# Kernel optimization log

Hardware: AMD Instinct MI355X
Metric: run time of the kernel (lower is better)

The kernel has to match this reference:

```python
import jax, jax.numpy as jnp
import numpy as np

B, L, D_ENC = 32, 512, 512
STEPS = 32
E_DIM = 128      # embedding_dim
A_DIM = 256      # attention_dim
H = 512          # hidden_size
VOCAB = 32000


def _linear(x, W, b):
    return x @ W.T + b


def setup_inputs() -> dict:
    key = jax.random.key(0)
    ks = jax.random.split(key, 12)
    s = lambda fan_in: 1.0 / np.sqrt(fan_in)
    return {
        "encoder_outputs": jax.random.normal(ks[0], (B, L, D_ENC), dtype=jnp.float32),
        "target_seq": jax.random.randint(ks[1], (B, STEPS), 0, VOCAB, dtype=jnp.int64),
        "pos_embedding": jax.random.normal(ks[2], (STEPS, E_DIM), dtype=jnp.float32),
        "dec_proj_W": jax.random.uniform(ks[3], (A_DIM, E_DIM), minval=-s(E_DIM), maxval=s(E_DIM)),
        "dec_proj_b": jnp.zeros((A_DIM,), jnp.float32),
        "enc_proj_W": jax.random.uniform(ks[4], (A_DIM, D_ENC), minval=-s(D_ENC), maxval=s(D_ENC)),
        "enc_proj_b": jnp.zeros((A_DIM,), jnp.float32),
        "attn_score_W": jax.random.uniform(ks[5], (1, A_DIM), minval=-s(A_DIM), maxval=s(A_DIM)),
        "attn_score_b": jnp.zeros((1,), jnp.float32),
        "hidden_proj_W": jax.random.uniform(ks[6], (H, E_DIM), minval=-s(E_DIM), maxval=s(E_DIM)),
        "hidden_proj_b": jnp.zeros((H,), jnp.float32),
        "fc_out_W": jax.random.uniform(ks[7], (VOCAB, H + D_ENC), minval=-s(H + D_ENC), maxval=s(H + D_ENC)),
        "fc_out_b": jnp.zeros((VOCAB,), jnp.float32),
    }


def reference(encoder_outputs, target_seq, pos_embedding,
              dec_proj_W, dec_proj_b, enc_proj_W, enc_proj_b,
              attn_score_W, attn_score_b, hidden_proj_W, hidden_proj_b,
              fc_out_W, fc_out_b):
    batch = encoder_outputs.shape[0]
    steps = target_seq.shape[1]
    # [B, L, A]
    enc_proj = _linear(encoder_outputs, enc_proj_W, enc_proj_b)
    # [B, S, E]  (dropout=0 in eval)
    pos_emb = jnp.broadcast_to(pos_embedding[:steps][None], (batch, steps, pos_embedding.shape[1]))
    # [B, S, A]
    dec_query = _linear(pos_emb, dec_proj_W, dec_proj_b)
    # additive attention: [B, S, L, A]
    combined = jnp.tanh(enc_proj[:, None, :, :] + dec_query[:, :, None, :])
    # score reduction to scalar: [B, S, L]
    attn_scores = jnp.einsum('bsla,a->bsl', combined, attn_score_W[0]) + attn_score_b[0]
    attn_weights = jax.nn.softmax(attn_scores, axis=2)
    # context: [B, S, D_enc]
    context = jnp.einsum('bsl,bld->bsd', attn_weights, encoder_outputs)
    hidden = _linear(pos_emb, hidden_proj_W, hidden_proj_b)  # [B, S, H]
    logits = _linear(jnp.concatenate([hidden, context], axis=-1), fc_out_W, fc_out_b)
    return logits
```

## Files before the change

kernel.cpp:

```cpp
#include <hip/hip_runtime.h>
#include <hip/hip_bf16.h>
#include <stdint.h>

typedef __attribute__((ext_vector_type(4))) float f32x4;
typedef __attribute__((ext_vector_type(8))) short short8;

#define B_   32
#define L_   512
#define DE_  512
#define S_   32
#define ED_  128
#define AD_  256
#define HD_  512
#define VOC_ 32000
#define M_   1024

__device__ __forceinline__ unsigned short f2bf(float f){
  union { float f; unsigned int u; } v; v.f = f;
  unsigned int u = v.u;
  unsigned int r = (u + 0x7FFFu + ((u >> 16) & 1u)) >> 16;
  return (unsigned short)r;
}

__device__ __forceinline__ float bf2f(unsigned short u){
  union { unsigned int u; float f; } v; v.u = ((unsigned int)u) << 16;
  return v.f;
}

__device__ __forceinline__ float tanh_fast(float x){
  float t = __expf(2.0f * x);
  return (t - 1.0f) * __builtin_amdgcn_rcpf(t + 1.0f);
}

__device__ __forceinline__ void gl_lds16(const void* g, void* l){
  __builtin_amdgcn_global_load_lds(
      (const __attribute__((address_space(1))) unsigned int*)g,
      (__attribute__((address_space(3))) unsigned int*)l, 16, 0, 0);
}

extern "C" __global__ void __launch_bounds__(256)
k_prep(const float* __restrict__ enc, unsigned short* __restrict__ enc_bf,
       const float* __restrict__ eW, unsigned short* __restrict__ encW_bf,
       const float* __restrict__ pos,
       const float* __restrict__ dW, const float* __restrict__ db,
       const float* __restrict__ hW, const float* __restrict__ hb,
       float* __restrict__ dq, unsigned short* __restrict__ hbf){
  int blk = blockIdx.x, tid = threadIdx.x;
  if (blk < 8192){
    int i = blk * 256 + tid;
    f32x4 v = ((const f32x4*)enc)[i];
    ushort4 o;
    o.x = f2bf(v[0]); o.y = f2bf(v[1]); o.z = f2bf(v[2]); o.w = f2bf(v[3]);
    ((ushort4*)enc_bf)[i] = o;
  } else if (blk < 8320){
    int i = (blk - 8192) * 256 + tid;
    f32x4 v = ((const f32x4*)eW)[i];
    ushort4 o;
    o.x = f2bf(v[0]); o.y = f2bf(v[1]); o.z = f2bf(v[2]); o.w = f2bf(v[3]);
    ((ushort4*)encW_bf)[i] = o;
  } else {
    int t = (blk - 8320) * 256 + tid;
    if (t < S_ * AD_){
      int s = t >> 8, a = t & 255;
      const float* p = pos + s * ED_;
      const float* wrow = dW + a * ED_;
      float acc = db[a];
      #pragma unroll 4
      for (int e = 0; e < ED_; ++e) acc += p[e] * wrow[e];
      dq[t] = acc;
    } else if (t < S_ * AD_ + S_ * HD_){
      int u = t - S_ * AD_;
      int s = u >> 9, h = u & 511;
      const float* p = pos + s * ED_;
      const float* wrow = hW + h * ED_;
      float acc = hb[h];
      #pragma unroll 4
      for (int e = 0; e < ED_; ++e) acc += p[e] * wrow[e];
      hbf[u] = f2bf(acc);
    }
  }
}

extern "C" __global__ void __launch_bounds__(256, 4)
k_gemm_encp(const unsigned short* __restrict__ A, const unsigned short* __restrict__ Bt,
            const float* __restrict__ bias, unsigned short* __restrict__ C){
  __shared__ unsigned short As[2][128 * 32];
  __shared__ unsigned short Bs[2][128 * 32];
  int bm = blockIdx.x >> 1, bn = blockIdx.x & 1;
  int tid = threadIdx.x, wid = tid >> 6, lane = tid & 63;
  int fr = lane & 15, fq = lane >> 4;
  int wm = wid >> 1, wn = wid & 1;
  int srow = lane >> 2;
  int scol = ((lane & 3) ^ ((lane >> 3) & 3)) * 8;
  int c0 = wid * 2;
  const unsigned short* aS0 = A  + (size_t)(bm * 128 + c0 * 16 + srow) * 512 + scol;
  const unsigned short* aS1 = aS0 + (size_t)16 * 512;
  const unsigned short* bS0 = Bt + (size_t)(bn * 128 + c0 * 16 + srow) * 512 + scol;
  const unsigned short* bS1 = bS0 + (size_t)16 * 512;
  int swzfq = (fq ^ ((fr >> 1) & 3)) * 8;

  f32x4 acc[4][4];
  #pragma unroll
  for (int i = 0; i < 4; ++i)
    #pragma unroll
    for (int j = 0; j < 4; ++j) acc[i][j] = (f32x4)0.0f;

#define STAGE_E(buf, kk) do { \
    gl_lds16(aS0 + (kk), &As[buf][c0 * 512]); \
    gl_lds16(aS1 + (kk), &As[buf][c0 * 512 + 512]); \
    gl_lds16(bS0 + (kk), &Bs[buf][c0 * 512]); \
    gl_lds16(bS1 + (kk), &Bs[buf][c0 * 512 + 512]); \
  } while (0)

  STAGE_E(0, 0);
  __syncthreads();

  int cur = 0;
  for (int t = 0; t < 16; ++t){
    if (t < 15) STAGE_E(cur ^ 1, (size_t)(t + 1) * 32);
    short8 a[4], b[4];
    #pragma unroll
    for (int mf = 0; mf < 4; ++mf) a[mf] = *(const short8*)&As[cur][(wm * 64 + mf * 16 + fr) * 32 + swzfq];
    #pragma unroll
    for (int nf = 0; nf < 4; ++nf) b[nf] = *(const short8*)&Bs[cur][(wn * 64 + nf * 16 + fr) * 32 + swzfq];
    #pragma unroll
    for (int mf = 0; mf < 4; ++mf)
      #pragma unroll
      for (int nf = 0; nf < 4; ++nf)
        acc[mf][nf] = __builtin_amdgcn_mfma_f32_16x16x32_bf16(a[mf], b[nf], acc[mf][nf], 0, 0, 0);
    __syncthreads();
    cur ^= 1;
  }
#undef STAGE_E

  #pragma unroll
  for (int mf = 0; mf < 4; ++mf){
    int row = bm * 128 + wm * 64 + mf * 16 + fq * 4;
    #pragma unroll
    for (int nf = 0; nf < 4; ++nf){
      int col = bn * 128 + wn * 64 + nf * 16 + fr;
      float bv = bias[col];
      #pragma unroll
      for (int j = 0; j < 4; ++j)
        C[(size_t)(row + j) * 256 + col] = f2bf(acc[mf][nf][j] + bv);
    }
  }
}

extern "C" __global__ void __launch_bounds__(256)
k_mid(const float* __restrict__ fcW, const unsigned short* __restrict__ hbf,
      const float* __restrict__ fcb, unsigned short* __restrict__ Wc,
      float* __restrict__ logh,
      const unsigned short* __restrict__ encp, const float* __restrict__ dq,
      const float* __restrict__ vW, float* __restrict__ wgt){
  int blk = blockIdx.x;
  if (blk < 500){
    int bn = blk;
    int tid = threadIdx.x, wid = tid >> 6, lane = tid & 63;
    int fr = lane & 15, fq = lane >> 4;
    #pragma unroll 8
    for (int i = 0; i < 32; ++i){
      int idx = i * 256 + tid;
      int row = idx >> 7, c4 = idx & 127;
      f32x4 v = *(const f32x4*)&fcW[(size_t)(bn * 64 + row) * 1024 + 512 + c4 * 4];
      ushort4 o;
      o.x = f2bf(v[0]); o.y = f2bf(v[1]); o.z = f2bf(v[2]); o.w = f2bf(v[3]);
      *(ushort4*)&Wc[(size_t)(bn * 64 + row) * 512 + c4 * 4] = o;
    }
    int col = bn * 64 + wid * 16 + fr;
    const float* brow = fcW + (size_t)col * 1024;
    f32x4 acc0 = (f32x4)0.0f, acc1 = (f32x4)0.0f;
    #pragma unroll 4
    for (int k0 = 0; k0 < 512; k0 += 32){
      int ko = k0 + fq * 8;
      f32x4 b0 = *(const f32x4*)(brow + ko);
      f32x4 b1 = *(const f32x4*)(brow + ko + 4);
      short8 bfr;
      bfr[0] = (short)f2bf(b0[0]); bfr[1] = (short)f2bf(b0[1]);
      bfr[2] = (short)f2bf(b0[2]); bfr[3] = (short)f2bf(b0[3]);
      bfr[4] = (short)f2bf(b1[0]); bfr[5] = (short)f2bf(b1[1]);
      bfr[6] = (short)f2bf(b1[2]); bfr[7] = (short)f2bf(b1[3]);
      short8 a0 = *(const short8*)&hbf[(size_t)fr * 512 + ko];
      short8 a1 = *(const short8*)&hbf[(size_t)(16 + fr) * 512 + ko];
      acc0 = __builtin_amdgcn_mfma_f32_16x16x32_bf16(a0, bfr, acc0, 0, 0, 0);
      acc1 = __builtin_amdgcn_mfma_f32_16x16x32_bf16(a1, bfr, acc1, 0, 0, 0);
    }
    float bv = fcb[col];
    #pragma unroll
    for (int j = 0; j < 4; ++j){
      logh[(size_t)(fq * 4 + j) * VOC_ + col]      = acc0[j] + bv;
      logh[(size_t)(16 + fq * 4 + j) * VOC_ + col] = acc1[j] + bv;
    }
  } else {
    int wg = blk - 500;
    int b = wg >> 5, s = wg & 31;
    int tid = threadIdx.x, wid = tid >> 6, lane = tid & 63;
    int half = lane >> 5, a0 = (lane & 31) * 8;
    __shared__ float sc[512];
    __shared__ float redm[4], reds[4];
    f32x4 dqa = *(const f32x4*)&dq[s * AD_ + a0];
    f32x4 dqb = *(const f32x4*)&dq[s * AD_ + a0 + 4];
    f32x4 va  = *(const f32x4*)&vW[a0];
    f32x4 vb  = *(const f32x4*)&vW[a0 + 4];
    for (int it = 0; it < 64; ++it){
      int l = wid * 128 + it * 2 + half;
      short8 e8 = *(const short8*)&encp[((size_t)(b * 512 + l)) * 256 + a0];
      float p = 0.0f;
      #pragma unroll
      for (int j = 0; j < 4; ++j) p += tanh_fast(bf2f((unsigned short)e8[j]) + dqa[j]) * va[j];
      #pragma unroll
      for (int j = 0; j < 4; ++j) p += tanh_fast(bf2f((unsigned short)e8[4 + j]) + dqb[j]) * vb[j];
      #pragma unroll
      for (int off = 16; off >= 1; off >>= 1) p += __shfl_xor(p, off);
      if ((lane & 31) == 0) sc[l] = p;
    }
    __syncthreads();
    float s0 = sc[tid], s1 = sc[tid + 256];
    float m = fmaxf(s0, s1);
    #pragma unroll
    for (int off = 32; off >= 1; off >>= 1) m = fmaxf(m, __shfl_xor(m, off));
    if (lane == 0) redm[wid] = m;
    __syncthreads();
    m = fmaxf(fmaxf(redm[0], redm[1]), fmaxf(redm[2], redm[3]));
    float e0 = __expf(s0 - m), e1 = __expf(s1 - m);
    float sum = e0 + e1;
    #pragma unroll
    for (int off = 32; off >= 1; off >>= 1) sum += __shfl_xor(sum, off);
    if (lane == 0) reds[wid] = sum;
    __syncthreads();
    float tot = reds[0] + reds[1] + reds[2] + reds[3];
    float inv = __builtin_amdgcn_rcpf(tot);
    size_t base = (size_t)(b * 32 + s) * 512;
    wgt[base + tid] = e0 * inv;
    wgt[base + tid + 256] = e1 * inv;
  }
}

extern "C" __global__ void __launch_bounds__(256)
k_ctx(const unsigned short* __restrict__ encb, const float* __restrict__ wgt,
      unsigned short* __restrict__ ctx){
  int b = blockIdx.x >> 4, dt = blockIdx.x & 15;
  int tid = threadIdx.x;
  __shared__ float wl[32 * 512];
  #pragma unroll 8
  for (int i = 0; i < 64; ++i)
    wl[i * 256 + tid] = wgt[(size_t)b * 16384 + i * 256 + tid];
  __syncthreads();
  int d = dt * 32 + (tid & 31);
  int grp = tid >> 5;
  float acc0 = 0, acc1 = 0, acc2 = 0, acc3 = 0;
  const unsigned short* ebase = encb + (size_t)b * 262144 + d;
  const float* w0 = &wl[(grp * 4 + 0) * 512];
  const float* w1 = &wl[(grp * 4 + 1) * 512];
  const float* w2 = &wl[(grp * 4 + 2) * 512];
  const float* w3 = &wl[(grp * 4 + 3) * 512];
  #pragma unroll 8
  for (int l = 0; l < 512; ++l){
    float e = bf2f(ebase[(size_t)l * 512]);
    acc0 += w0[l] * e; acc1 += w1[l] * e; acc2 += w2[l] * e; acc3 += w3[l] * e;
  }
  size_t obase = (size_t)(b * 32 + grp * 4) * 512 + d;
  ctx[obase]        = f2bf(acc0);
  ctx[obase + 512]  = f2bf(acc1);
  ctx[obase + 1024] = f2bf(acc2);
  ctx[obase + 1536] = f2bf(acc3);
}

extern "C" __global__ void __launch_bounds__(512, 4)
k_gemm_main(const unsigned short* __restrict__ Abf, const unsigned short* __restrict__ Wc,
            const float* __restrict__ logh, float* __restrict__ out){
  __shared__ unsigned short As[2][128 * 32];
  __shared__ unsigned short Bs[3][256 * 32];
  int orig = blockIdx.x;
  int wg = (orig & 7) * 125 + (orig >> 3);
  int bm = wg & 7, bn = wg >> 3;
  int tid = threadIdx.x, wid = tid >> 6, lane = tid & 63;
  int fr = lane & 15, fq = lane >> 4;
  int wm = wid >> 2, wn = wid & 3;
  int abase = bm * 128, bbase = bn * 256;
  int srow = lane >> 2;
  int scol = ((lane & 3) ^ ((lane >> 3) & 3)) * 8;
  const unsigned short* aS0 = Abf + (size_t)(abase + wid * 16 + srow) * 512 + scol;
  const unsigned short* bS0 = Wc  + (size_t)(bbase + wid * 32 + srow) * 512 + scol;
  const unsigned short* bS1 = bS0 + (size_t)16 * 512;
  int swzfq = (fq ^ ((fr >> 1) & 3)) * 8;

  f32x4 acc[4][4];
  #pragma unroll
  for (int i = 0; i < 4; ++i)
    #pragma unroll
    for (int jj = 0; jj < 4; ++jj) acc[i][jj] = (f32x4)0.0f;

#define STAGE_A(buf, kk) gl_lds16(aS0 + (kk), &As[buf][wid * 512])
#define STAGE_B(buf, kk) do { \
    gl_lds16(bS0 + (kk), &Bs[buf][wid * 1024]); \
    gl_lds16(bS1 + (kk), &Bs[buf][wid * 1024 + 512]); \
  } while (0)

  STAGE_A(0, 0);
  STAGE_B(0, 0);
  STAGE_B(1, 32);
  asm volatile("s_waitcnt vmcnt(2)" ::: "memory");
  __builtin_amdgcn_s_barrier();
  __builtin_amdgcn_sched_barrier(0);

  #pragma unroll
  for (int t = 0; t < 16; ++t){
    const int ca = t & 1, cb = t % 3;
    short8 a[4], b[4];
    if (t < 15) STAGE_A(ca ^ 1, (size_t)(t + 1) * 32);
    #pragma unroll
    for (int nf = 0; nf < 4; ++nf)
      b[nf] = *(const short8*)&Bs[cb][(wn * 64 + nf * 16 + fr) * 32 + swzfq];
    #pragma unroll
    for (int mf = 0; mf < 2; ++mf)
      a[mf] = *(const short8*)&As[ca][(wm * 64 + mf * 16 + fr) * 32 + swzfq];
    __builtin_amdgcn_s_setprio(1);
    #pragma unroll
    for (int mf = 0; mf < 2; ++mf)
      #pragma unroll
      for (int nf = 0; nf < 4; ++nf)
        acc[mf][nf] = __builtin_amdgcn_mfma_f32_16x16x32_bf16(a[mf], b[nf], acc[mf][nf], 0, 0, 0);
    __builtin_amdgcn_s_setprio(0);
    if (t < 14) STAGE_B((t + 2) % 3, (size_t)(t + 2) * 32);
    #pragma unroll
    for (int mf = 2; mf < 4; ++mf)
      a[mf] = *(const short8*)&As[ca][(wm * 64 + mf * 16 + fr) * 32 + swzfq];
    __builtin_amdgcn_s_setprio(1);
    #pragma unroll
    for (int mf = 2; mf < 4; ++mf)
      #pragma unroll
      for (int nf = 0; nf < 4; ++nf)
        acc[mf][nf] = __builtin_amdgcn_mfma_f32_16x16x32_bf16(a[mf], b[nf], acc[mf][nf], 0, 0, 0);
    __builtin_amdgcn_s_setprio(0);
    if (t < 14)       asm volatile("s_waitcnt vmcnt(2)" ::: "memory");
    else if (t == 14) asm volatile("s_waitcnt vmcnt(0)" ::: "memory");
    if (t < 15){
      __builtin_amdgcn_s_barrier();
      __builtin_amdgcn_sched_barrier(0);
    }
  }
#undef STAGE_A
#undef STAGE_B

  #pragma unroll
  for (int mf = 0; mf < 4; ++mf){
    int rowb = bm * 128 + wm * 64 + mf * 16 + fq * 4;
    #pragma unroll
    for (int nf = 0; nf < 4; ++nf){
      int col = bn * 256 + wn * 64 + nf * 16 + fr;
      #pragma unroll
      for (int jj = 0; jj < 4; ++jj){
        int r = rowb + jj;
        out[(size_t)r * VOC_ + col] = acc[mf][nf][jj] + logh[(size_t)(r & 31) * VOC_ + col];
      }
    }
  }
}

extern "C" void kernel_launch(void* const* d_in, const int* in_sizes, int n_in,
                              void* d_out, int out_size, void* d_ws, size_t ws_size,
                              hipStream_t stream){
  const float* enc = (const float*)d_in[0];
  const float* pos = (const float*)d_in[2];
  const float* dW  = (const float*)d_in[3];
  const float* db  = (const float*)d_in[4];
  const float* eW  = (const float*)d_in[5];
  const float* eb  = (const float*)d_in[6];
  const float* vW  = (const float*)d_in[7];
  const float* hW  = (const float*)d_in[9];
  const float* hb  = (const float*)d_in[10];
  const float* fcW = (const float*)d_in[11];
  const float* fcb = (const float*)d_in[12];
  float* out = (float*)d_out;

  char* w = (char*)d_ws;
  unsigned short* Wc_bf   = (unsigned short*)(w);
  unsigned short* enc_bf  = (unsigned short*)(w + 32768000);
  unsigned short* encp_bf = (unsigned short*)(w + 49545216);
  unsigned short* ctx     = (unsigned short*)(w + 57933824);
  float*          logh    = (float*)(w + 58982400);
  float*          dq      = (float*)(w + 63078400);
  unsigned short* hbf     = (unsigned short*)(w + 63111168);
  unsigned short* encW_bf = (unsigned short*)(w + 63143936);
  float*          wgt     = (float*)(w + 63406080);

  k_prep<<<dim3(8416), dim3(256), 0, stream>>>(enc, enc_bf, eW, encW_bf,
                                               pos, dW, db, hW, hb, dq, hbf);
  k_gemm_encp<<<dim3(256), dim3(256), 0, stream>>>(enc_bf, encW_bf, eb, encp_bf);
  k_mid<<<dim3(1524), dim3(256), 0, stream>>>(fcW, hbf, fcb, Wc_bf, logh,
                                              encp_bf, dq, vW, wgt);
  k_ctx<<<dim3(512), dim3(256), 0, stream>>>(enc_bf, wgt, ctx);
  k_gemm_main<<<dim3(1000), dim3(512), 0, stream>>>(ctx, Wc_bf, logh, out);
}
```

Baseline: 204.5 us.

## Tile attention scores over L-chunks with LDS reuse and split softmax into separate kernel

```diff
diff --git a/kernel.cpp b/kernel.cpp
--- a/kernel.cpp
+++ b/kernel.cpp
@@ -152,7 +152,8 @@
       const float* __restrict__ fcb, unsigned short* __restrict__ Wc,
       float* __restrict__ logh,
       const unsigned short* __restrict__ encp, const float* __restrict__ dq,
-      const float* __restrict__ vW, float* __restrict__ wgt){
+      const float* __restrict__ vW, float* __restrict__ scoreT){
+  __shared__ char smem[49152];
   int blk = blockIdx.x;
   if (blk < 500){
     int bn = blk;
@@ -192,47 +193,88 @@
       logh[(size_t)(16 + fq * 4 + j) * VOC_ + col] = acc1[j] + bv;
     }
   } else {
-    int wg = blk - 500;
-    int b = wg >> 5, s = wg & 31;
-    int tid = threadIdx.x, wid = tid >> 6, lane = tid & 63;
-    int half = lane >> 5, a0 = (lane & 31) * 8;
-    __shared__ float sc[512];
-    __shared__ float redm[4], reds[4];
-    f32x4 dqa = *(const f32x4*)&dq[s * AD_ + a0];
-    f32x4 dqb = *(const f32x4*)&dq[s * AD_ + a0 + 4];
-    f32x4 va  = *(const f32x4*)&vW[a0];
-    f32x4 vb  = *(const f32x4*)&vW[a0 + 4];
-    for (int it = 0; it < 64; ++it){
-      int l = wid * 128 + it * 2 + half;
-      short8 e8 = *(const short8*)&encp[((size_t)(b * 512 + l)) * 256 + a0];
-      float p = 0.0f;
-      #pragma unroll
-      for (int j = 0; j < 4; ++j) p += tanh_fast(bf2f((unsigned short)e8[j]) + dqa[j]) * va[j];
-      #pragma unroll
-      for (int j = 0; j < 4; ++j) p += tanh_fast(bf2f((unsigned short)e8[4 + j]) + dqb[j]) * vb[j];
-      #pragma unroll
-      for (int off = 16; off >= 1; off >>= 1) p += __shfl_xor(p, off);
-      if ((lane & 31) == 0) sc[l] = p;
+    unsigned short* eL = (unsigned short*)smem;
+    float* pp = (float*)(smem + 16384);
+    int blk2 = blk - 500;
+    int b = blk2 >> 4, c = blk2 & 15;
+    int tid = threadIdx.x, w = tid >> 6, lane = tid & 63;
+    #pragma unroll
+    for (int i = 0; i < 4; ++i){
+      int rb = i * 8 + w * 2;
+      gl_lds16(encp + (size_t)(b * 512 + c * 32 + rb + (lane >> 5)) * 256 + (lane & 31) * 8,
+               &eL[rb * 256]);
+    }
+    int s = tid >> 3, g = tid & 7;
+    f32x4 dqv[8], vv[8];
+    #pragma unroll
+    for (int k = 0; k < 8; ++k){
+      dqv[k] = *(const f32x4*)&dq[s * 256 + g * 32 + k * 4];
+      vv[k]  = *(const f32x4*)&vW[g * 32 + k * 4];
     }
     __syncthreads();
-    float s0 = sc[tid], s1 = sc[tid + 256];
-    float m = fmaxf(s0, s1);
-    #pragma unroll
-    for (int off = 32; off >= 1; off >>= 1) m = fmaxf(m, __shfl_xor(m, off));
-    if (lane == 0) redm[wid] = m;
+    #pragma unroll 4
+    for (int l = 0; l < 32; ++l){
+      float a = 0.0f;
+      #pragma unroll
+      for (int k = 0; k < 8; ++k){
+        uint2 e4 = *(const uint2*)&eL[l * 256 + g * 32 + k * 4];
+        a += tanh_fast(bf2f((unsigned short)(e4.x & 0xffff)) + dqv[k][0]) * vv[k][0];
+        a += tanh_fast(bf2f((unsigned short)(e4.x >> 16))    + dqv[k][1]) * vv[k][1];
+        a += tanh_fast(bf2f((unsigned short)(e4.y & 0xffff)) + dqv[k][2]) * vv[k][2];
+        a += tanh_fast(bf2f((unsigned short)(e4.y >> 16))    + dqv[k][3]) * vv[k][3];
+      }
+      pp[l * 256 + tid] = a;
+    }
     __syncthreads();
-    m = fmaxf(fmaxf(redm[0], redm[1]), fmaxf(redm[2], redm[3]));
-    float e0 = __expf(s0 - m), e1 = __expf(s1 - m);
-    float sum = e0 + e1;
-    #pragma unroll
-    for (int off = 32; off >= 1; off >>= 1) sum += __shfl_xor(sum, off);
-    if (lane == 0) reds[wid] = sum;
-    __syncthreads();
-    float tot = reds[0] + reds[1] + reds[2] + reds[3];
-    float inv = __builtin_amdgcn_rcpf(tot);
-    size_t base = (size_t)(b * 32 + s) * 512;
-    wgt[base + tid] = e0 * inv;
-    wgt[base + tid + 256] = e1 * inv;
+    #pragma unroll
+    for (int k2 = 0; k2 < 4; ++k2){
+      int p = tid + k2 * 256;
+      int l = p >> 5, ss = p & 31;
+      f32x4 x0 = *(const f32x4*)&pp[p * 8];
+      f32x4 x1 = *(const f32x4*)&pp[p * 8 + 4];
+      float sum = (x0[0] + x0[1]) + (x0[2] + x0[3]) + ((x1[0] + x1[1]) + (x1[2] + x1[3]));
+      scoreT[((size_t)b * 512 + c * 32 + l) * 32 + ss] = sum;
+    }
+  }
+}
+
+extern "C" __global__ void __launch_bounds__(256)
+k_smax(const float* __restrict__ scoreT, float* __restrict__ wgt){
+  __shared__ float sL[512 * 32];
+  __shared__ float pm[32][8], ps[32][8];
+  __shared__ float Mf[32], invf[32];
+  int b = blockIdx.x, tid = threadIdx.x;
+  for (int idx = tid; idx < 16384; idx += 256){
+    int l = idx >> 5, s2 = idx & 31;
+    sL[l * 32 + (s2 ^ (l & 31))] = scoreT[(size_t)b * 16384 + idx];
+  }
+  __syncthreads();
+  int s2 = tid & 31, part = tid >> 5;
+  float m = -1e30f;
+  for (int l = part * 64; l < part * 64 + 64; ++l)
+    m = fmaxf(m, sL[l * 32 + (s2 ^ (l & 31))]);
+  pm[s2][part] = m;
+  __syncthreads();
+  float M = pm[s2][0];
+  #pragma unroll
+  for (int j2 = 1; j2 < 8; ++j2) M = fmaxf(M, pm[s2][j2]);
+  float sum = 0.0f;
+  for (int l = part * 64; l < part * 64 + 64; ++l)
+    sum += __expf(sL[l * 32 + (s2 ^ (l & 31))] - M);
+  ps[s2][part] = sum;
+  __syncthreads();
+  if (part == 0){
+    float L = ps[s2][0];
+    #pragma unroll
+    for (int j2 = 1; j2 < 8; ++j2) L += ps[s2][j2];
+    Mf[s2] = M;
+    invf[s2] = __builtin_amdgcn_rcpf(L);
+  }
+  __syncthreads();
+  for (int idx = tid; idx < 16384; idx += 256){
+    int ss = idx >> 9, l = idx & 511;
+    float x = sL[l * 32 + (ss ^ (l & 31))];
+    wgt[(size_t)(b * 32 + ss) * 512 + l] = __expf(x - Mf[ss]) * invf[ss];
   }
 }
 
@@ -384,12 +426,14 @@
   unsigned short* hbf     = (unsigned short*)(w + 63111168);
   unsigned short* encW_bf = (unsigned short*)(w + 63143936);
   float*          wgt     = (float*)(w + 63406080);
+  float*          scoreT  = (float*)(w + 65503232);
 
   k_prep<<<dim3(8416), dim3(256), 0, stream>>>(enc, enc_bf, eW, encW_bf,
                                                pos, dW, db, hW, hb, dq, hbf);
   k_gemm_encp<<<dim3(256), dim3(256), 0, stream>>>(enc_bf, encW_bf, eb, encp_bf);
-  k_mid<<<dim3(1524), dim3(256), 0, stream>>>(fcW, hbf, fcb, Wc_bf, logh,
-                                              encp_bf, dq, vW, wgt);
+  k_mid<<<dim3(1012), dim3(256), 0, stream>>>(fcW, hbf, fcb, Wc_bf, logh,
+                                              encp_bf, dq, vW, scoreT);
+  k_smax<<<dim3(32), dim3(256), 0, stream>>>(scoreT, wgt);
   k_ctx<<<dim3(512), dim3(256), 0, stream>>>(enc_bf, wgt, ctx);
   k_gemm_main<<<dim3(1000), dim3(512), 0, stream>>>(ctx, Wc_bf, logh, out);
 }
```

Result: slower. 218.0 us (+6.6%).
